# Kernel optimization log

Measured on AMD Instinct MI355X. Metric: run time of the kernel, lower is better.

## Reference

```python
import jax, jax.numpy as jnp
import numpy as np

N_USER = 250_000
N_ITEM = 250_000
E = 500_000
IN, H, C = 128, 64, 2
NEG_SLOPE = 0.01  # torch F.leaky_relu default


def setup_inputs() -> dict:
    key = jax.random.key(0)
    ks = jax.random.split(key, 24)
    d = {}
    d["feat_user"] = jax.random.normal(ks[0], (N_USER, IN), jnp.float32)
    d["feat_item"] = jax.random.normal(ks[1], (N_ITEM, IN), jnp.float32)
    # per-etype linear params, layer 1 (in_feats -> h_dim)
    s1 = 1.0 / np.sqrt(IN)
    d["W1_follows"] = jax.random.normal(ks[2], (IN, H), jnp.float32) * s1
    d["b1_follows"] = jax.random.normal(ks[3], (H,), jnp.float32) * s1
    d["W1_clicks"]  = jax.random.normal(ks[4], (IN, H), jnp.float32) * s1
    d["b1_clicks"]  = jax.random.normal(ks[5], (H,), jnp.float32) * s1
    d["W1_rev"]     = jax.random.normal(ks[6], (IN, H), jnp.float32) * s1
    d["b1_rev"]     = jax.random.normal(ks[7], (H,), jnp.float32) * s1
    # per-etype linear params, layer 2 (h_dim -> num_classes)
    s2 = 1.0 / np.sqrt(H)
    d["W2_follows"] = jax.random.normal(ks[8], (H, C), jnp.float32) * s2
    d["b2_follows"] = jax.random.normal(ks[9], (C,), jnp.float32) * s2
    d["W2_clicks"]  = jax.random.normal(ks[10], (H, C), jnp.float32) * s2
    d["b2_clicks"]  = jax.random.normal(ks[11], (C,), jnp.float32) * s2
    d["W2_rev"]     = jax.random.normal(ks[12], (H, C), jnp.float32) * s2
    d["b2_rev"]     = jax.random.normal(ks[13], (C,), jnp.float32) * s2
    # edge lists: (src, dst) per canonical etype
    d["follows_src"] = jax.random.randint(ks[14], (E,), 0, N_USER, jnp.int32)  # user->user
    d["follows_dst"] = jax.random.randint(ks[15], (E,), 0, N_USER, jnp.int32)
    d["clicks_src"]  = jax.random.randint(ks[16], (E,), 0, N_USER, jnp.int32)  # user->item
    d["clicks_dst"]  = jax.random.randint(ks[17], (E,), 0, N_ITEM, jnp.int32)
    d["rev_src"]     = jax.random.randint(ks[18], (E,), 0, N_ITEM, jnp.int32)  # item->user
    d["rev_dst"]     = jax.random.randint(ks[19], (E,), 0, N_USER, jnp.int32)
    return d


def _mean_agg(Wh, src, dst, n_dst):
    # copy_u + mean: gather transformed src feats per edge, segment-mean onto dst
    m = Wh[src]                                                   # [E, d]
    s = jax.ops.segment_sum(m, dst, num_segments=n_dst)           # [n_dst, d]
    deg = jax.ops.segment_sum(jnp.ones_like(dst, Wh.dtype), dst, num_segments=n_dst)
    return s / jnp.maximum(deg, 1.0)[:, None]                     # 0 for deg-0 nodes (DGL fills 0)


def _layer(fu, fi, Wf, bf, Wc, bc, Wr, br,
           fsrc, fdst, csrc, cdst, rsrc, rdst):
    # per-etype linear on src features, per-etype mean, cross-etype 'sum'
    h_user = (_mean_agg(fu @ Wf + bf, fsrc, fdst, N_USER)
              + _mean_agg(fi @ Wr + br, rsrc, rdst, N_USER))
    h_item = _mean_agg(fu @ Wc + bc, csrc, cdst, N_ITEM)
    return h_user, h_item


def reference(feat_user, feat_item,
              W1_follows, b1_follows, W1_clicks, b1_clicks, W1_rev, b1_rev,
              W2_follows, b2_follows, W2_clicks, b2_clicks, W2_rev, b2_rev,
              follows_src, follows_dst, clicks_src, clicks_dst, rev_src, rev_dst):
    h1u, h1i = _layer(feat_user, feat_item,
                      W1_follows, b1_follows, W1_clicks, b1_clicks, W1_rev, b1_rev,
                      follows_src, follows_dst, clicks_src, clicks_dst, rev_src, rev_dst)
    h2u = jnp.where(h1u >= 0, h1u, NEG_SLOPE * h1u)
    h2i = jnp.where(h1i >= 0, h1i, NEG_SLOPE * h1i)
    out_u, out_i = _layer(h2u, h2i,
                          W2_follows, b2_follows, W2_clicks, b2_clicks, W2_rev, b2_rev,
                          follows_src, follows_dst, clicks_src, clicks_dst, rev_src, rev_dst)
    # (h_dict, h_dict_2) flattened per ntype
    return (out_u, out_i, h2u, h2i)
```

## Files before the change

kernel.cpp:

```cpp
#include <hip/hip_runtime.h>
#include <cstdio>

#define NU 250000
#define NI 250000
#define NE 500000
#define ND 250000
#define NB_SCAN 245
#define NR 8
#define RSZ 31250

typedef __attribute__((ext_vector_type(8))) short short8v;
typedef __attribute__((ext_vector_type(4))) float float4v;

__device__ inline unsigned short f2bf(float x) {
  unsigned int b = __float_as_uint(x);
  unsigned int r = (b + 0x7FFFu + ((b >> 16) & 1u)) >> 16;
  return (unsigned short)r;
}
__device__ inline float bf2f(unsigned short u) {
  return __uint_as_float(((unsigned int)u) << 16);
}

__device__ inline void async_copy16(const float* g, float* l) {
  __builtin_amdgcn_global_load_lds((const __attribute__((address_space(1))) void*)g,
                                   (__attribute__((address_space(3))) void*)l, 16, 0, 0);
}

__global__ void hist3_kernel(const int* __restrict__ fdst, const int* __restrict__ cdst,
                             const int* __restrict__ rdst,
                             int* __restrict__ degf, int* __restrict__ degc, int* __restrict__ degr) {
  int i = blockIdx.x * blockDim.x + threadIdx.x;
  if (i < NE) {
    atomicAdd(&degf[fdst[i]], 1);
    atomicAdd(&degc[cdst[i]], 1);
    atomicAdd(&degr[rdst[i]], 1);
  }
}

__global__ void scan1_kernel(const int* __restrict__ deg0, const int* __restrict__ deg1,
                             const int* __restrict__ deg2, int* __restrict__ bsum) {
  const int* deg = blockIdx.y == 0 ? deg0 : (blockIdx.y == 1 ? deg1 : deg2);
  int* bs = bsum + blockIdx.y * 256;
  __shared__ int s[256];
  int b = blockIdx.x, t = threadIdx.x;
  int base = b * 1024 + t * 4;
  int v = 0;
  #pragma unroll
  for (int i = 0; i < 4; ++i) if (base + i < ND) v += deg[base + i];
  s[t] = v; __syncthreads();
  for (int off = 128; off > 0; off >>= 1) { if (t < off) s[t] += s[t + off]; __syncthreads(); }
  if (t == 0) bs[b] = s[0];
}

__global__ void scan2_kernel(int* __restrict__ bsum) {
  int* bs = bsum + blockIdx.x * 256;
  __shared__ int s[256];
  int t = threadIdx.x;
  s[t] = (t < NB_SCAN) ? bs[t] : 0;
  __syncthreads();
  for (int off = 1; off < 256; off <<= 1) {
    int x = (t >= off) ? s[t - off] : 0;
    __syncthreads();
    s[t] += x;
    __syncthreads();
  }
  if (t < NB_SCAN) bs[t] = (t == 0) ? 0 : s[t - 1];
}

__global__ void scan3_kernel(const int* __restrict__ deg0, const int* __restrict__ deg1,
                             const int* __restrict__ deg2, const int* __restrict__ bsum,
                             int* __restrict__ offs0, int* __restrict__ offs1, int* __restrict__ offs2,
                             int* __restrict__ cur0, int* __restrict__ cur1, int* __restrict__ cur2) {
  int y = blockIdx.y;
  const int* deg = y == 0 ? deg0 : (y == 1 ? deg1 : deg2);
  int* offs = y == 0 ? offs0 : (y == 1 ? offs1 : offs2);
  int* cursor = y == 0 ? cur0 : (y == 1 ? cur1 : cur2);
  const int* bs = bsum + y * 256;
  __shared__ int s[256];
  int b = blockIdx.x, t = threadIdx.x;
  int base = b * 1024 + t * 4;
  int v[4]; int sum = 0;
  #pragma unroll
  for (int i = 0; i < 4; ++i) { v[i] = (base + i < ND) ? deg[base + i] : 0; sum += v[i]; }
  s[t] = sum; __syncthreads();
  for (int off = 1; off < 256; off <<= 1) {
    int x = (t >= off) ? s[t - off] : 0;
    __syncthreads();
    s[t] += x;
    __syncthreads();
  }
  int run = bs[b] + s[t] - sum;
  #pragma unroll
  for (int i = 0; i < 4; ++i) {
    if (base + i < ND) { offs[base + i] = run; cursor[base + i] = run; run += v[i]; }
  }
  if (b == 0 && t == 0) offs[ND] = NE;
}

__global__ void bucket_part_kernel(const int* __restrict__ fsrc, const int* __restrict__ fdst,
                                   const int* __restrict__ csrc, const int* __restrict__ cdst,
                                   const int* __restrict__ rsrc, const int* __restrict__ rdst,
                                   int* __restrict__ curf, int* __restrict__ curc, int* __restrict__ curr,
                                   int* __restrict__ srtf, int* __restrict__ srtc, int* __restrict__ srtr) {
  const int r = blockIdx.x & (NR - 1);
  const int chunk = blockIdx.x >> 3;
  const int lo = r * RSZ, hi = lo + RSZ;
  const int base = chunk * 1024;
  #pragma unroll
  for (int i = 0; i < 4; ++i) {
    int e = base + i * 256 + threadIdx.x;
    if (e < NE) {
      int d0 = fdst[e]; int s0 = fsrc[e];
      if (d0 >= lo && d0 < hi) { int p = atomicAdd(&curf[d0], 1); srtf[p] = s0; }
      int d1 = cdst[e]; int s1 = csrc[e];
      if (d1 >= lo && d1 < hi) { int p = atomicAdd(&curc[d1], 1); srtc[p] = s1; }
      int d2 = rdst[e]; int s2 = rsrc[e];
      if (d2 >= lo && d2 < hi) { int p = atomicAdd(&curr[d2], 1); srtr[p] = s2; }
    }
  }
}

__global__ void prepw_kernel(const float* __restrict__ W0, const float* __restrict__ W1,
                             const float* __restrict__ W2, unsigned short* __restrict__ T) {
  int gt = blockIdx.x * 256 + threadIdx.x;
  int et = gt >> 10;
  int g = gt & 1023;
  int gl = g & 63;
  int jm = (g >> 6) & 3;
  int c = g >> 8;
  int kb = c * 32 + (gl >> 4) * 8;
  int col = jm * 16 + (gl & 15);
  const float* W = et == 0 ? W0 : (et == 1 ? W1 : W2);
  short8v u;
  #pragma unroll
  for (int i = 0; i < 8; ++i) u[i] = (short)f2bf(W[(kb + i) * 64 + col]);
  ((short8v*)T)[gt] = u;
}

template <bool TWO>
__global__ __launch_bounds__(256, 2) void gemm_dma_kernel(
    const float* __restrict__ X, int n, int ntiles,
    const unsigned short* __restrict__ Ta, const float* __restrict__ ba,
    const unsigned short* __restrict__ Tb, const float* __restrict__ bb,
    unsigned short* __restrict__ Ya, unsigned short* __restrict__ Yb) {
  __shared__ float sx[2][64 * 128];
  const int tid = threadIdx.x;
  const int lane = tid & 63;
  const int wave = tid >> 6;
  const int cb = (lane >> 4) * 4;

  short8v A[4][4], B[4][4];
  #pragma unroll
  for (int c = 0; c < 4; ++c) {
    #pragma unroll
    for (int jm = 0; jm < 4; ++jm) {
      A[c][jm] = ((const short8v*)Ta)[c * 256 + jm * 64 + lane];
      if constexpr (TWO) B[c][jm] = ((const short8v*)Tb)[c * 256 + jm * 64 + lane];
    }
  }
  float4 bias_a[4], bias_b[4];
  #pragma unroll
  for (int jm = 0; jm < 4; ++jm) {
    bias_a[jm] = *(const float4*)&ba[jm * 16 + cb];
    if constexpr (TWO) bias_b[jm] = *(const float4*)&bb[jm * 16 + cb];
  }

  const int nl = wave * 16 + (lane & 15);
  const int sw = nl & 7;

  int t = blockIdx.x;
  {
    #pragma unroll
    for (int j = 0; j < 8; ++j) {
      int idx = (wave * 8 + j) * 64 + lane;
      int row = idx >> 5, u = idx & 31;
      int gr = t * 64 + row; if (gr >= n) gr = n - 1;
      const float* src = X + (size_t)gr * 128 + ((u ^ (row & 7)) << 2);
      float* dst = &sx[0][(wave * 8 + j) * 256];
      async_copy16(src, dst);
    }
  }
  asm volatile("s_waitcnt vmcnt(0)" ::: "memory");
  __syncthreads();

  int cur = 0;
  while (true) {
    int tn = t + (int)gridDim.x;
    bool more = (tn < ntiles);
    if (more) {
      #pragma unroll
      for (int j = 0; j < 8; ++j) {
        int idx = (wave * 8 + j) * 64 + lane;
        int row = idx >> 5, u = idx & 31;
        int gr = tn * 64 + row; if (gr >= n) gr = n - 1;
        const float* src = X + (size_t)gr * 128 + ((u ^ (row & 7)) << 2);
        float* dst = &sx[cur ^ 1][(wave * 8 + j) * 256];
        async_copy16(src, dst);
      }
    }

    float4v accA[4] = {};
    float4v accB[4] = {};
    #pragma unroll
    for (int c = 0; c < 4; ++c) {
      int s0 = c * 8 + (lane >> 4) * 2;
      float4 f0 = *(const float4*)&sx[cur][nl * 128 + (((s0 + 0) ^ sw) << 2)];
      float4 f1 = *(const float4*)&sx[cur][nl * 128 + (((s0 + 1) ^ sw) << 2)];
      short8v bfr;
      bfr[0] = (short)f2bf(f0.x); bfr[1] = (short)f2bf(f0.y);
      bfr[2] = (short)f2bf(f0.z); bfr[3] = (short)f2bf(f0.w);
      bfr[4] = (short)f2bf(f1.x); bfr[5] = (short)f2bf(f1.y);
      bfr[6] = (short)f2bf(f1.z); bfr[7] = (short)f2bf(f1.w);
      #pragma unroll
      for (int jm = 0; jm < 4; ++jm) {
        accA[jm] = __builtin_amdgcn_mfma_f32_16x16x32_bf16(A[c][jm], bfr, accA[jm], 0, 0, 0);
        if constexpr (TWO)
          accB[jm] = __builtin_amdgcn_mfma_f32_16x16x32_bf16(B[c][jm], bfr, accB[jm], 0, 0, 0);
      }
    }
    int node = t * 64 + nl;
    if (node < n) {
      #pragma unroll
      for (int jm = 0; jm < 4; ++jm) {
        ushort4 o;
        o.x = f2bf(accA[jm][0] + bias_a[jm].x);
        o.y = f2bf(accA[jm][1] + bias_a[jm].y);
        o.z = f2bf(accA[jm][2] + bias_a[jm].z);
        o.w = f2bf(accA[jm][3] + bias_a[jm].w);
        *(ushort4*)&Ya[(size_t)node * 64 + jm * 16 + cb] = o;
        if constexpr (TWO) {
          ushort4 o2;
          o2.x = f2bf(accB[jm][0] + bias_b[jm].x);
          o2.y = f2bf(accB[jm][1] + bias_b[jm].y);
          o2.z = f2bf(accB[jm][2] + bias_b[jm].z);
          o2.w = f2bf(accB[jm][3] + bias_b[jm].w);
          *(ushort4*)&Yb[(size_t)node * 64 + jm * 16 + cb] = o2;
        }
      }
    }

    if (!more) break;
    asm volatile("s_waitcnt vmcnt(0)" ::: "memory");
    __syncthreads();
    cur ^= 1;
    t = tn;
  }
}

__global__ __launch_bounds__(256) void agg_fused_kernel(
    const unsigned short* __restrict__ Whf, const unsigned short* __restrict__ Whr,
    const unsigned short* __restrict__ Whc,
    const int* __restrict__ offs_f, const int* __restrict__ srt_f,
    const int* __restrict__ offs_r, const int* __restrict__ srt_r,
    const int* __restrict__ offs_c, const int* __restrict__ srt_c,
    const float* __restrict__ W2f, const float* __restrict__ b2f,
    const float* __restrict__ W2c, const float* __restrict__ b2c,
    const float* __restrict__ W2r, const float* __restrict__ b2r,
    float* __restrict__ h2u, float* __restrict__ h2i,
    float* __restrict__ Y2f, float* __restrict__ Y2c, float* __restrict__ Y2r,
    int ub) {
  const int tid = threadIdx.x;
  const int gid = tid >> 4;
  const int q = tid & 15;

  if (blockIdx.x < ub) {
    int d0 = (blockIdx.x * 16 + gid) * 2;
    int d1 = d0 + 1;
    bool v0 = d0 < NU, v1 = d1 < NU;
    int ef0 = v0 ? offs_f[d0] : 0, ef0e = v0 ? offs_f[d0 + 1] : 0;
    int ef1 = v1 ? offs_f[d1] : 0, ef1e = v1 ? offs_f[d1 + 1] : 0;
    int er0 = v0 ? offs_r[d0] : 0, er0e = v0 ? offs_r[d0 + 1] : 0;
    int er1 = v1 ? offs_r[d1] : 0, er1e = v1 ? offs_r[d1 + 1] : 0;
    float rf0 = 1.0f / fmaxf((float)(ef0e - ef0), 1.0f);
    float rf1 = 1.0f / fmaxf((float)(ef1e - ef1), 1.0f);
    float rr0 = 1.0f / fmaxf((float)(er0e - er0), 1.0f);
    float rr1 = 1.0f / fmaxf((float)(er1e - er1), 1.0f);

    float af0[4] = {0, 0, 0, 0}, af1[4] = {0, 0, 0, 0};
    float ar0[4] = {0, 0, 0, 0}, ar1[4] = {0, 0, 0, 0};
    while (ef0 < ef0e || ef1 < ef1e || er0 < er0e || er1 < er1e) {
      bool hf0 = ef0 < ef0e, hf1 = ef1 < ef1e, hr0 = er0 < er0e, hr1 = er1 < er1e;
      ushort4 vf0, vf1, vr0, vr1;
      if (hf0) { int s = srt_f[ef0]; vf0 = *(const ushort4*)&Whf[(size_t)s * 64 + q * 4]; }
      if (hf1) { int s = srt_f[ef1]; vf1 = *(const ushort4*)&Whf[(size_t)s * 64 + q * 4]; }
      if (hr0) { int s = srt_r[er0]; vr0 = *(const ushort4*)&Whr[(size_t)s * 64 + q * 4]; }
      if (hr1) { int s = srt_r[er1]; vr1 = *(const ushort4*)&Whr[(size_t)s * 64 + q * 4]; }
      if (hf0) { af0[0] += bf2f(vf0.x); af0[1] += bf2f(vf0.y); af0[2] += bf2f(vf0.z); af0[3] += bf2f(vf0.w); ++ef0; }
      if (hf1) { af1[0] += bf2f(vf1.x); af1[1] += bf2f(vf1.y); af1[2] += bf2f(vf1.z); af1[3] += bf2f(vf1.w); ++ef1; }
      if (hr0) { ar0[0] += bf2f(vr0.x); ar0[1] += bf2f(vr0.y); ar0[2] += bf2f(vr0.z); ar0[3] += bf2f(vr0.w); ++er0; }
      if (hr1) { ar1[0] += bf2f(vr1.x); ar1[1] += bf2f(vr1.y); ar1[2] += bf2f(vr1.z); ar1[3] += bf2f(vr1.w); ++er1; }
    }

    float h0v[4], h1v[4];
    #pragma unroll
    for (int i = 0; i < 4; ++i) {
      float x0 = af0[i] * rf0 + ar0[i] * rr0;
      h0v[i] = x0 >= 0.f ? x0 : 0.01f * x0;
      float x1 = af1[i] * rf1 + ar1[i] * rr1;
      h1v[i] = x1 >= 0.f ? x1 : 0.01f * x1;
    }
    if (v0) *(float4*)&h2u[(size_t)d0 * 64 + q * 4] = make_float4(h0v[0], h0v[1], h0v[2], h0v[3]);
    if (v1) *(float4*)&h2u[(size_t)d1 * 64 + q * 4] = make_float4(h1v[0], h1v[1], h1v[2], h1v[3]);

    float pf00 = 0, pf01 = 0, pc00 = 0, pc01 = 0;
    float pf10 = 0, pf11 = 0, pc10 = 0, pc11 = 0;
    #pragma unroll
    for (int i = 0; i < 4; ++i) {
      int j = q * 4 + i;
      float wf0 = W2f[j * 2 + 0], wf1 = W2f[j * 2 + 1];
      float wc0 = W2c[j * 2 + 0], wc1 = W2c[j * 2 + 1];
      pf00 += h0v[i] * wf0; pf01 += h0v[i] * wf1;
      pc00 += h0v[i] * wc0; pc01 += h0v[i] * wc1;
      pf10 += h1v[i] * wf0; pf11 += h1v[i] * wf1;
      pc10 += h1v[i] * wc0; pc11 += h1v[i] * wc1;
    }
    #pragma unroll
    for (int off = 1; off < 16; off <<= 1) {
      pf00 += __shfl_xor(pf00, off, 64); pf01 += __shfl_xor(pf01, off, 64);
      pc00 += __shfl_xor(pc00, off, 64); pc01 += __shfl_xor(pc01, off, 64);
      pf10 += __shfl_xor(pf10, off, 64); pf11 += __shfl_xor(pf11, off, 64);
      pc10 += __shfl_xor(pc10, off, 64); pc11 += __shfl_xor(pc11, off, 64);
    }
    if (q == 0) {
      if (v0) {
        Y2f[(size_t)d0 * 2 + 0] = pf00 + b2f[0]; Y2f[(size_t)d0 * 2 + 1] = pf01 + b2f[1];
        Y2c[(size_t)d0 * 2 + 0] = pc00 + b2c[0]; Y2c[(size_t)d0 * 2 + 1] = pc01 + b2c[1];
      }
      if (v1) {
        Y2f[(size_t)d1 * 2 + 0] = pf10 + b2f[0]; Y2f[(size_t)d1 * 2 + 1] = pf11 + b2f[1];
        Y2c[(size_t)d1 * 2 + 0] = pc10 + b2c[0]; Y2c[(size_t)d1 * 2 + 1] = pc11 + b2c[1];
      }
    }
  } else {
    int d0 = ((blockIdx.x - ub) * 16 + gid) * 2;
    int d1 = d0 + 1;
    bool v0 = d0 < NI, v1 = d1 < NI;
    int ec0 = v0 ? offs_c[d0] : 0, ec0e = v0 ? offs_c[d0 + 1] : 0;
    int ec1 = v1 ? offs_c[d1] : 0, ec1e = v1 ? offs_c[d1 + 1] : 0;
    float rc0 = 1.0f / fmaxf((float)(ec0e - ec0), 1.0f);
    float rc1 = 1.0f / fmaxf((float)(ec1e - ec1), 1.0f);

    float ac0[4] = {0, 0, 0, 0}, ac1[4] = {0, 0, 0, 0};
    while (ec0 < ec0e || ec1 < ec1e) {
      bool h0 = ec0 < ec0e, h1 = ec1 < ec1e;
      ushort4 v0v, v1v;
      if (h0) { int s = srt_c[ec0]; v0v = *(const ushort4*)&Whc[(size_t)s * 64 + q * 4]; }
      if (h1) { int s = srt_c[ec1]; v1v = *(const ushort4*)&Whc[(size_t)s * 64 + q * 4]; }
      if (h0) { ac0[0] += bf2f(v0v.x); ac0[1] += bf2f(v0v.y); ac0[2] += bf2f(v0v.z); ac0[3] += bf2f(v0v.w); ++ec0; }
      if (h1) { ac1[0] += bf2f(v1v.x); ac1[1] += bf2f(v1v.y); ac1[2] += bf2f(v1v.z); ac1[3] += bf2f(v1v.w); ++ec1; }
    }

    float h0v[4], h1v[4];
    #pragma unroll
    for (int i = 0; i < 4; ++i) {
      float x0 = ac0[i] * rc0;
      h0v[i] = x0 >= 0.f ? x0 : 0.01f * x0;
      float x1 = ac1[i] * rc1;
      h1v[i] = x1 >= 0.f ? x1 : 0.01f * x1;
    }
    if (v0) *(float4*)&h2i[(size_t)d0 * 64 + q * 4] = make_float4(h0v[0], h0v[1], h0v[2], h0v[3]);
    if (v1) *(float4*)&h2i[(size_t)d1 * 64 + q * 4] = make_float4(h1v[0], h1v[1], h1v[2], h1v[3]);

    float p00 = 0, p01 = 0, p10 = 0, p11 = 0;
    #pragma unroll
    for (int i = 0; i < 4; ++i) {
      int j = q * 4 + i;
      float w0 = W2r[j * 2 + 0], w1 = W2r[j * 2 + 1];
      p00 += h0v[i] * w0; p01 += h0v[i] * w1;
      p10 += h1v[i] * w0; p11 += h1v[i] * w1;
    }
    #pragma unroll
    for (int off = 1; off < 16; off <<= 1) {
      p00 += __shfl_xor(p00, off, 64); p01 += __shfl_xor(p01, off, 64);
      p10 += __shfl_xor(p10, off, 64); p11 += __shfl_xor(p11, off, 64);
    }
    if (q == 0) {
      if (v0) { Y2r[(size_t)d0 * 2 + 0] = p00 + b2r[0]; Y2r[(size_t)d0 * 2 + 1] = p01 + b2r[1]; }
      if (v1) { Y2r[(size_t)d1 * 2 + 0] = p10 + b2r[0]; Y2r[(size_t)d1 * 2 + 1] = p11 + b2r[1]; }
    }
  }
}

__global__ void out_fused_kernel(const float* __restrict__ Y2f, const float* __restrict__ Y2r,
                                 const float* __restrict__ Y2c,
                                 const int* __restrict__ offs_f, const int* __restrict__ srt_f,
                                 const int* __restrict__ offs_r, const int* __restrict__ srt_r,
                                 const int* __restrict__ offs_c, const int* __restrict__ srt_c,
                                 float* __restrict__ out_u, float* __restrict__ out_i, int ub) {
  if (blockIdx.x < ub) {
    int d = blockIdx.x * 256 + threadIdx.x;
    if (d >= NU) return;
    int f = offs_f[d], f1 = offs_f[d + 1];
    int r = offs_r[d], r1 = offs_r[d + 1];
    float rf = 1.0f / fmaxf((float)(f1 - f), 1.0f);
    float rr = 1.0f / fmaxf((float)(r1 - r), 1.0f);
    float a0 = 0.f, a1 = 0.f, c0 = 0.f, c1 = 0.f;
    while (f < f1 || r < r1) {
      bool hf = f < f1, hr = r < r1;
      float2 yf, yr;
      if (hf) { int s = srt_f[f]; yf = *(const float2*)&Y2f[(size_t)s * 2]; }
      if (hr) { int s = srt_r[r]; yr = *(const float2*)&Y2r[(size_t)s * 2]; }
      if (hf) { a0 += yf.x; a1 += yf.y; ++f; }
      if (hr) { c0 += yr.x; c1 += yr.y; ++r; }
    }
    out_u[(size_t)d * 2 + 0] = a0 * rf + c0 * rr;
    out_u[(size_t)d * 2 + 1] = a1 * rf + c1 * rr;
  } else {
    int d = (blockIdx.x - ub) * 256 + threadIdx.x;
    if (d >= NI) return;
    int c = offs_c[d], c1e = offs_c[d + 1];
    float rc = 1.0f / fmaxf((float)(c1e - c), 1.0f);
    float a0 = 0.f, a1 = 0.f;
    for (; c < c1e; ++c) {
      int s = srt_c[c];
      a0 += Y2c[(size_t)s * 2 + 0]; a1 += Y2c[(size_t)s * 2 + 1];
    }
    out_i[(size_t)d * 2 + 0] = a0 * rc;
    out_i[(size_t)d * 2 + 1] = a1 * rc;
  }
}

extern "C" void kernel_launch(void* const* d_in, const int* in_sizes, int n_in,
                              void* d_out, int out_size, void* d_ws, size_t ws_size,
                              hipStream_t stream) {
  const float* feat_user = (const float*)d_in[0];
  const float* feat_item = (const float*)d_in[1];
  const float* W1f = (const float*)d_in[2];  const float* b1f = (const float*)d_in[3];
  const float* W1c = (const float*)d_in[4];  const float* b1c = (const float*)d_in[5];
  const float* W1r = (const float*)d_in[6];  const float* b1r = (const float*)d_in[7];
  const float* W2f = (const float*)d_in[8];  const float* b2f = (const float*)d_in[9];
  const float* W2c = (const float*)d_in[10]; const float* b2c = (const float*)d_in[11];
  const float* W2r = (const float*)d_in[12]; const float* b2r = (const float*)d_in[13];
  const int* fsrc = (const int*)d_in[14];  const int* fdst = (const int*)d_in[15];
  const int* csrc = (const int*)d_in[16];  const int* cdst = (const int*)d_in[17];
  const int* rsrc = (const int*)d_in[18];  const int* rdst = (const int*)d_in[19];

  float* out = (float*)d_out;
  float* out_u = out;
  float* out_i = out + 2 * NU;
  float* h2u  = out + 1000000;
  float* h2i  = out + 17000000;

  unsigned short* Whf = (unsigned short*)d_ws;
  unsigned short* Whc = Whf + 16000000;
  unsigned short* Whr = Whc + 16000000;
  unsigned short* Wtab = Whr + 16000000;
  unsigned short* Tf = Wtab;
  unsigned short* Tc = Wtab + 8192;
  unsigned short* Tr = Wtab + 16384;
  int* ibase = (int*)(Wtab + 24576);
  const int P = 250304;
  int* offs_f = ibase;            int* offs_c = offs_f + P;  int* offs_r = offs_c + P;
  int* cur_f  = offs_r + P;       int* cur_c  = cur_f + P;   int* cur_r  = cur_c + P;
  int* deg_f  = cur_r + P;        int* deg_c  = deg_f + P;   int* deg_r  = deg_c + P;
  int* srt_f  = deg_r + P;
  int* srt_c  = srt_f + 500096;
  int* srt_r  = srt_c + 500096;
  int* bsum   = srt_r + 500096;
  float* Y2f  = (float*)(bsum + 768);
  float* Y2c  = Y2f + 500000;
  float* Y2r  = Y2c + 500000;

  size_t need = 96000000ull + 24576ull * 2ull
              + (9ull * P + 3ull * 500096ull + 768ull + 1500000ull) * 4ull;
  if (ws_size < need) {
    fprintf(stderr, "kernel_launch: ws too small (%zu < %zu)\n", ws_size, need);
    return;
  }

  hipMemsetAsync(deg_f, 0, (size_t)(3 * P) * 4, stream);

  const int eb = (NE + 255) / 256;

  prepw_kernel<<<12, 256, 0, stream>>>(W1f, W1c, W1r, Wtab);

  const int utiles = (NU + 63) / 64;
  const int itiles = (NI + 63) / 64;
  gemm_dma_kernel<true><<<512, 256, 0, stream>>>(feat_user, NU, utiles, Tf, b1f, Tc, b1c, Whf, Whc);
  gemm_dma_kernel<false><<<512, 256, 0, stream>>>(feat_item, NI, itiles, Tr, b1r, nullptr, nullptr, Whr, nullptr);

  hist3_kernel<<<eb, 256, 0, stream>>>(fdst, cdst, rdst, deg_f, deg_c, deg_r);
  scan1_kernel<<<dim3(NB_SCAN, 3), 256, 0, stream>>>(deg_f, deg_c, deg_r, bsum);
  scan2_kernel<<<3, 256, 0, stream>>>(bsum);
  scan3_kernel<<<dim3(NB_SCAN, 3), 256, 0, stream>>>(deg_f, deg_c, deg_r, bsum,
                                                     offs_f, offs_c, offs_r,
                                                     cur_f, cur_c, cur_r);
  const int chunks = (NE + 1023) / 1024;
  bucket_part_kernel<<<chunks * NR, 256, 0, stream>>>(fsrc, fdst, csrc, cdst, rsrc, rdst,
                                                      cur_f, cur_c, cur_r, srt_f, srt_c, srt_r);

  const int ub = (NU + 31) / 32;
  agg_fused_kernel<<<2 * ub, 256, 0, stream>>>(Whf, Whr, Whc,
                                               offs_f, srt_f, offs_r, srt_r, offs_c, srt_c,
                                               W2f, b2f, W2c, b2c, W2r, b2r,
                                               h2u, h2i, Y2f, Y2c, Y2r, ub);

  const int ob = (NU + 255) / 256;
  out_fused_kernel<<<2 * ob, 256, 0, stream>>>(Y2f, Y2r, Y2c,
                                               offs_f, srt_f, offs_r, srt_r, offs_c, srt_c,
                                               out_u, out_i, ob);
}
```

Baseline: 344.7 us.

## Fuse layer-1 GEMMs with histogram and bucketing kernels via block-range split

```diff
diff --git a/kernel.cpp b/kernel.cpp
--- a/kernel.cpp
+++ b/kernel.cpp
@@ -8,6 +8,9 @@
 #define NB_SCAN 245
 #define NR 8
 #define RSZ 31250
+#define HB 1954
+#define BB 3912
+#define GT 3907
 
 typedef __attribute__((ext_vector_type(8))) short short8v;
 typedef __attribute__((ext_vector_type(4))) float float4v;
@@ -26,14 +29,129 @@
                                    (__attribute__((address_space(3))) void*)l, 16, 0, 0);
 }
 
-__global__ void hist3_kernel(const int* __restrict__ fdst, const int* __restrict__ cdst,
-                             const int* __restrict__ rdst,
-                             int* __restrict__ degf, int* __restrict__ degc, int* __restrict__ degr) {
-  int i = blockIdx.x * blockDim.x + threadIdx.x;
-  if (i < NE) {
-    atomicAdd(&degf[fdst[i]], 1);
-    atomicAdd(&degc[cdst[i]], 1);
-    atomicAdd(&degr[rdst[i]], 1);
+template <bool TWO>
+__device__ inline void gemm_tile(int t, const float* __restrict__ X, int n,
+                                 const unsigned short* __restrict__ Ta, const float* __restrict__ ba,
+                                 const unsigned short* __restrict__ Tb, const float* __restrict__ bb,
+                                 unsigned short* __restrict__ Ya, unsigned short* __restrict__ Yb) {
+  __shared__ float sx[64 * 128];
+  const int tid = threadIdx.x;
+  const int lane = tid & 63;
+  const int wave = tid >> 6;
+
+  #pragma unroll
+  for (int j = 0; j < 8; ++j) {
+    int idx = (wave * 8 + j) * 64 + lane;
+    int row = idx >> 5, u = idx & 31;
+    int gr = t * 64 + row; if (gr >= n) gr = n - 1;
+    const float* src = X + (size_t)gr * 128 + ((u ^ (row & 7)) << 2);
+    float* dst = &sx[(wave * 8 + j) * 256];
+    async_copy16(src, dst);
+  }
+  asm volatile("s_waitcnt vmcnt(0)" ::: "memory");
+  __syncthreads();
+
+  const int nl = wave * 16 + (lane & 15);
+  const int sw = nl & 7;
+  const int cb = (lane >> 4) * 4;
+
+  float4v accA[4] = {};
+  float4v accB[4] = {};
+  #pragma unroll
+  for (int c = 0; c < 4; ++c) {
+    short8v a[4], a2[4];
+    #pragma unroll
+    for (int jm = 0; jm < 4; ++jm) {
+      a[jm] = ((const short8v*)Ta)[c * 256 + jm * 64 + lane];
+      if constexpr (TWO) a2[jm] = ((const short8v*)Tb)[c * 256 + jm * 64 + lane];
+    }
+    int s0 = c * 8 + (lane >> 4) * 2;
+    float4 f0 = *(const float4*)&sx[nl * 128 + (((s0 + 0) ^ sw) << 2)];
+    float4 f1 = *(const float4*)&sx[nl * 128 + (((s0 + 1) ^ sw) << 2)];
+    short8v bfr;
+    bfr[0] = (short)f2bf(f0.x); bfr[1] = (short)f2bf(f0.y);
+    bfr[2] = (short)f2bf(f0.z); bfr[3] = (short)f2bf(f0.w);
+    bfr[4] = (short)f2bf(f1.x); bfr[5] = (short)f2bf(f1.y);
+    bfr[6] = (short)f2bf(f1.z); bfr[7] = (short)f2bf(f1.w);
+    #pragma unroll
+    for (int jm = 0; jm < 4; ++jm) {
+      accA[jm] = __builtin_amdgcn_mfma_f32_16x16x32_bf16(a[jm], bfr, accA[jm], 0, 0, 0);
+      if constexpr (TWO)
+        accB[jm] = __builtin_amdgcn_mfma_f32_16x16x32_bf16(a2[jm], bfr, accB[jm], 0, 0, 0);
+    }
+  }
+
+  int node = t * 64 + nl;
+  if (node < n) {
+    #pragma unroll
+    for (int jm = 0; jm < 4; ++jm) {
+      float4 bias = *(const float4*)&ba[jm * 16 + cb];
+      ushort4 o;
+      o.x = f2bf(accA[jm][0] + bias.x);
+      o.y = f2bf(accA[jm][1] + bias.y);
+      o.z = f2bf(accA[jm][2] + bias.z);
+      o.w = f2bf(accA[jm][3] + bias.w);
+      *(ushort4*)&Ya[(size_t)node * 64 + jm * 16 + cb] = o;
+      if constexpr (TWO) {
+        float4 bias2 = *(const float4*)&bb[jm * 16 + cb];
+        ushort4 o2;
+        o2.x = f2bf(accB[jm][0] + bias2.x);
+        o2.y = f2bf(accB[jm][1] + bias2.y);
+        o2.z = f2bf(accB[jm][2] + bias2.z);
+        o2.w = f2bf(accB[jm][3] + bias2.w);
+        *(ushort4*)&Yb[(size_t)node * 64 + jm * 16 + cb] = o2;
+      }
+    }
+  }
+}
+
+__global__ __launch_bounds__(256) void histF_gemmI_kernel(
+    const int* __restrict__ fdst, const int* __restrict__ cdst, const int* __restrict__ rdst,
+    int* __restrict__ degf, int* __restrict__ degc, int* __restrict__ degr,
+    const float* __restrict__ Xi,
+    const unsigned short* __restrict__ Tr, const float* __restrict__ b1r,
+    unsigned short* __restrict__ Whr) {
+  if (blockIdx.x < HB) {
+    int i = blockIdx.x * 256 + threadIdx.x;
+    if (i < NE) {
+      atomicAdd(&degf[fdst[i]], 1);
+      atomicAdd(&degc[cdst[i]], 1);
+      atomicAdd(&degr[rdst[i]], 1);
+    }
+  } else {
+    gemm_tile<false>(blockIdx.x - HB, Xi, NI, Tr, b1r, nullptr, nullptr, Whr, nullptr);
+  }
+}
+
+__global__ __launch_bounds__(256) void bucketF_gemmU_kernel(
+    const int* __restrict__ fsrc, const int* __restrict__ fdst,
+    const int* __restrict__ csrc, const int* __restrict__ cdst,
+    const int* __restrict__ rsrc, const int* __restrict__ rdst,
+    int* __restrict__ curf, int* __restrict__ curc, int* __restrict__ curr,
+    int* __restrict__ srtf, int* __restrict__ srtc, int* __restrict__ srtr,
+    const float* __restrict__ Xu,
+    const unsigned short* __restrict__ Tf, const float* __restrict__ b1f,
+    const unsigned short* __restrict__ Tc, const float* __restrict__ b1c,
+    unsigned short* __restrict__ Whf, unsigned short* __restrict__ Whc) {
+  if (blockIdx.x < BB) {
+    const int r = blockIdx.x & (NR - 1);
+    const int chunk = blockIdx.x >> 3;
+    const int lo = r * RSZ, hi = lo + RSZ;
+    const int base = chunk * 1024;
+    #pragma unroll
+    for (int i = 0; i < 4; ++i) {
+      int e = base + i * 256 + threadIdx.x;
+      if (e < NE) {
+        int d0 = fdst[e]; int s0 = fsrc[e];
+        if (d0 >= lo && d0 < hi) { int p = atomicAdd(&curf[d0], 1); srtf[p] = s0; }
+        int d1 = cdst[e]; int s1 = csrc[e];
+        if (d1 >= lo && d1 < hi) { int p = atomicAdd(&curc[d1], 1); srtc[p] = s1; }
+        int d2 = rdst[e]; int s2 = rsrc[e];
+        if (d2 >= lo && d2 < hi) { int p = atomicAdd(&curr[d2], 1); srtr[p] = s2; }
+      }
+    }
+  } else {
+    gemm_tile<true>(blockIdx.x - BB, Xu, NU, Tf, b1f, Tc, b1c, Whf, Whc);
   }
 }
 
@@ -97,29 +215,6 @@
   if (b == 0 && t == 0) offs[ND] = NE;
 }
 
-__global__ void bucket_part_kernel(const int* __restrict__ fsrc, const int* __restrict__ fdst,
-                                   const int* __restrict__ csrc, const int* __restrict__ cdst,
-                                   const int* __restrict__ rsrc, const int* __restrict__ rdst,
-                                   int* __restrict__ curf, int* __restrict__ curc, int* __restrict__ curr,
-                                   int* __restrict__ srtf, int* __restrict__ srtc, int* __restrict__ srtr) {
-  const int r = blockIdx.x & (NR - 1);
-  const int chunk = blockIdx.x >> 3;
-  const int lo = r * RSZ, hi = lo + RSZ;
-  const int base = chunk * 1024;
-  #pragma unroll
-  for (int i = 0; i < 4; ++i) {
-    int e = base + i * 256 + threadIdx.x;
-    if (e < NE) {
-      int d0 = fdst[e]; int s0 = fsrc[e];
-      if (d0 >= lo && d0 < hi) { int p = atomicAdd(&curf[d0], 1); srtf[p] = s0; }
-      int d1 = cdst[e]; int s1 = csrc[e];
-      if (d1 >= lo && d1 < hi) { int p = atomicAdd(&curc[d1], 1); srtc[p] = s1; }
-      int d2 = rdst[e]; int s2 = rsrc[e];
-      if (d2 >= lo && d2 < hi) { int p = atomicAdd(&curr[d2], 1); srtr[p] = s2; }
-    }
-  }
-}
-
 __global__ void prepw_kernel(const float* __restrict__ W0, const float* __restrict__ W1,
                              const float* __restrict__ W2, unsigned short* __restrict__ T) {
   int gt = blockIdx.x * 256 + threadIdx.x;
@@ -135,116 +230,6 @@
   #pragma unroll
   for (int i = 0; i < 8; ++i) u[i] = (short)f2bf(W[(kb + i) * 64 + col]);
   ((short8v*)T)[gt] = u;
-}
-
-template <bool TWO>
-__global__ __launch_bounds__(256, 2) void gemm_dma_kernel(
-    const float* __restrict__ X, int n, int ntiles,
-    const unsigned short* __restrict__ Ta, const float* __restrict__ ba,
-    const unsigned short* __restrict__ Tb, const float* __restrict__ bb,
-    unsigned short* __restrict__ Ya, unsigned short* __restrict__ Yb) {
-  __shared__ float sx[2][64 * 128];
-  const int tid = threadIdx.x;
-  const int lane = tid & 63;
-  const int wave = tid >> 6;
-  const int cb = (lane >> 4) * 4;
-
-  short8v A[4][4], B[4][4];
-  #pragma unroll
-  for (int c = 0; c < 4; ++c) {
-    #pragma unroll
-    for (int jm = 0; jm < 4; ++jm) {
-      A[c][jm] = ((const short8v*)Ta)[c * 256 + jm * 64 + lane];
-      if constexpr (TWO) B[c][jm] = ((const short8v*)Tb)[c * 256 + jm * 64 + lane];
-    }
-  }
-  float4 bias_a[4], bias_b[4];
-  #pragma unroll
-  for (int jm = 0; jm < 4; ++jm) {
-    bias_a[jm] = *(const float4*)&ba[jm * 16 + cb];
-    if constexpr (TWO) bias_b[jm] = *(const float4*)&bb[jm * 16 + cb];
-  }
-
-  const int nl = wave * 16 + (lane & 15);
-  const int sw = nl & 7;
-
-  int t = blockIdx.x;
-  {
-    #pragma unroll
-    for (int j = 0; j < 8; ++j) {
-      int idx = (wave * 8 + j) * 64 + lane;
-      int row = idx >> 5, u = idx & 31;
-      int gr = t * 64 + row; if (gr >= n) gr = n - 1;
-      const float* src = X + (size_t)gr * 128 + ((u ^ (row & 7)) << 2);
-      float* dst = &sx[0][(wave * 8 + j) * 256];
-      async_copy16(src, dst);
-    }
-  }
-  asm volatile("s_waitcnt vmcnt(0)" ::: "memory");
-  __syncthreads();
-
-  int cur = 0;
-  while (true) {
-    int tn = t + (int)gridDim.x;
-    bool more = (tn < ntiles);
-    if (more) {
-      #pragma unroll
-      for (int j = 0; j < 8; ++j) {
-        int idx = (wave * 8 + j) * 64 + lane;
-        int row = idx >> 5, u = idx & 31;
-        int gr = tn * 64 + row; if (gr >= n) gr = n - 1;
-        const float* src = X + (size_t)gr * 128 + ((u ^ (row & 7)) << 2);
-        float* dst = &sx[cur ^ 1][(wave * 8 + j) * 256];
-        async_copy16(src, dst);
-      }
-    }
-
-    float4v accA[4] = {};
-    float4v accB[4] = {};
-    #pragma unroll
-    for (int c = 0; c < 4; ++c) {
-      int s0 = c * 8 + (lane >> 4) * 2;
-      float4 f0 = *(const float4*)&sx[cur][nl * 128 + (((s0 + 0) ^ sw) << 2)];
-      float4 f1 = *(const float4*)&sx[cur][nl * 128 + (((s0 + 1) ^ sw) << 2)];
-      short8v bfr;
-      bfr[0] = (short)f2bf(f0.x); bfr[1] = (short)f2bf(f0.y);
-      bfr[2] = (short)f2bf(f0.z); bfr[3] = (short)f2bf(f0.w);
-      bfr[4] = (short)f2bf(f1.x); bfr[5] = (short)f2bf(f1.y);
-      bfr[6] = (short)f2bf(f1.z); bfr[7] = (short)f2bf(f1.w);
-      #pragma unroll
-      for (int jm = 0; jm < 4; ++jm) {
-        accA[jm] = __builtin_amdgcn_mfma_f32_16x16x32_bf16(A[c][jm], bfr, accA[jm], 0, 0, 0);
-        if constexpr (TWO)
-          accB[jm] = __builtin_amdgcn_mfma_f32_16x16x32_bf16(B[c][jm], bfr, accB[jm], 0, 0, 0);
-      }
-    }
-    int node = t * 64 + nl;
-    if (node < n) {
-      #pragma unroll
-      for (int jm = 0; jm < 4; ++jm) {
-        ushort4 o;
-        o.x = f2bf(accA[jm][0] + bias_a[jm].x);
-        o.y = f2bf(accA[jm][1] + bias_a[jm].y);
-        o.z = f2bf(accA[jm][2] + bias_a[jm].z);
-        o.w = f2bf(accA[jm][3] + bias_a[jm].w);
-        *(ushort4*)&Ya[(size_t)node * 64 + jm * 16 + cb] = o;
-        if constexpr (TWO) {
-          ushort4 o2;
-          o2.x = f2bf(accB[jm][0] + bias_b[jm].x);
-          o2.y = f2bf(accB[jm][1] + bias_b[jm].y);
-          o2.z = f2bf(accB[jm][2] + bias_b[jm].z);
-          o2.w = f2bf(accB[jm][3] + bias_b[jm].w);
-          *(ushort4*)&Yb[(size_t)node * 64 + jm * 16 + cb] = o2;
-        }
-      }
-    }
-
-    if (!more) break;
-    asm volatile("s_waitcnt vmcnt(0)" ::: "memory");
-    __syncthreads();
-    cur ^= 1;
-    t = tn;
-  }
 }
 
 __global__ __launch_bounds__(256) void agg_fused_kernel(
@@ -470,24 +455,20 @@
 
   hipMemsetAsync(deg_f, 0, (size_t)(3 * P) * 4, stream);
 
-  const int eb = (NE + 255) / 256;
-
   prepw_kernel<<<12, 256, 0, stream>>>(W1f, W1c, W1r, Wtab);
 
-  const int utiles = (NU + 63) / 64;
-  const int itiles = (NI + 63) / 64;
-  gemm_dma_kernel<true><<<512, 256, 0, stream>>>(feat_user, NU, utiles, Tf, b1f, Tc, b1c, Whf, Whc);
-  gemm_dma_kernel<false><<<512, 256, 0, stream>>>(feat_item, NI, itiles, Tr, b1r, nullptr, nullptr, Whr, nullptr);
-
-  hist3_kernel<<<eb, 256, 0, stream>>>(fdst, cdst, rdst, deg_f, deg_c, deg_r);
+  histF_gemmI_kernel<<<HB + GT, 256, 0, stream>>>(fdst, cdst, rdst, deg_f, deg_c, deg_r,
+                                                  feat_item, Tr, b1r, Whr);
+
   scan1_kernel<<<dim3(NB_SCAN, 3), 256, 0, stream>>>(deg_f, deg_c, deg_r, bsum);
   scan2_kernel<<<3, 256, 0, stream>>>(bsum);
   scan3_kernel<<<dim3(NB_SCAN, 3), 256, 0, stream>>>(deg_f, deg_c, deg_r, bsum,
                                                      offs_f, offs_c, offs_r,
                                                      cur_f, cur_c, cur_r);
-  const int chunks = (NE + 1023) / 1024;
-  bucket_part_kernel<<<chunks * NR, 256, 0, stream>>>(fsrc, fdst, csrc, cdst, rsrc, rdst,
-                                                      cur_f, cur_c, cur_r, srt_f, srt_c, srt_r);
+
+  bucketF_gemmU_kernel<<<BB + GT, 256, 0, stream>>>(fsrc, fdst, csrc, cdst, rsrc, rdst,
+                                                    cur_f, cur_c, cur_r, srt_f, srt_c, srt_r,
+                                                    feat_user, Tf, b1f, Tc, b1c, Whf, Whc);
 
   const int ub = (NU + 31) / 32;
   agg_fused_kernel<<<2 * ub, 256, 0, stream>>>(Whf, Whr, Whc,
```

New measurement: 348.1 us. About the same (+1.0%).
